# Kernel optimization log

Measured on AMD Instinct MI355X. Metric: run time of the kernel, lower is better.

The kernel has to match this reference:

```python
import jax, jax.numpy as jnp
import numpy as np

N = 8192        # batch_size == num nodes == num hyperedges
D = 512         # hidden_dim
H_HEADS = 8
HD = D // H_HEADS
TOP_K = 16
EPS = 1e-5      # LayerNorm eps


def setup_inputs() -> dict:
    key = jax.random.key(0)
    ks = jax.random.split(key, 10)
    def rn(k, shape, scale=0.02):
        return jax.random.normal(k, shape, dtype=jnp.float32) * scale
    return {
        "x0": jax.random.normal(ks[0], (N, D), dtype=jnp.float32),
        "x1": jax.random.normal(ks[1], (N, D), dtype=jnp.float32),
        # modality projections: Linear -> ReLU -> LayerNorm (per modality)
        "w_p0": rn(ks[2], (D, D)), "b_p0": jnp.zeros((D,), jnp.float32),
        "g0": jnp.ones((D,), jnp.float32), "beta0": jnp.zeros((D,), jnp.float32),
        "w_p1": rn(ks[3], (D, D)), "b_p1": jnp.zeros((D,), jnp.float32),
        "g1": jnp.ones((D,), jnp.float32), "beta1": jnp.zeros((D,), jnp.float32),
        # MultiheadAttention packed in-proj + out-proj
        "in_w": rn(ks[4], (3 * D, D)), "in_b": jnp.zeros((3 * D,), jnp.float32),
        "out_w": rn(ks[5], (D, D)), "out_b": jnp.zeros((D,), jnp.float32),
        # edge weight predictor MLP
        "ew_w1": rn(ks[6], (D // 2, D)), "ew_b1": jnp.zeros((D // 2,), jnp.float32),
        "ew_w2": rn(ks[7], (1, D // 2)), "ew_b2": jnp.zeros((1,), jnp.float32),
    }


def _layernorm(x, g, b):
    m = x.mean(-1, keepdims=True)
    v = ((x - m) ** 2).mean(-1, keepdims=True)
    return (x - m) * jax.lax.rsqrt(v + EPS) * g + b


def _forward(x0, x1, w_p0, b_p0, g0, beta0, w_p1, b_p1, g1, beta1,
             in_w, in_b, out_w, out_b, ew_w1, ew_b1, ew_w2, ew_b2):
    # per-modality projection: Linear -> ReLU -> LayerNorm
    p0 = _layernorm(jax.nn.relu(x0 @ w_p0.T + b_p0), g0, beta0)
    p1 = _layernorm(jax.nn.relu(x1 @ w_p1.T + b_p1), g1, beta1)
    seq = jnp.stack([p0, p1], axis=1)                       # [N, 2, D]
    # cross-modal MHA (self-attention over the 2 modality tokens)
    qkv = seq @ in_w.T + in_b                               # [N, 2, 3D]
    q, k, v = jnp.split(qkv, 3, axis=-1)
    q = q.reshape(N, 2, H_HEADS, HD)
    k = k.reshape(N, 2, H_HEADS, HD)
    v = v.reshape(N, 2, H_HEADS, HD)
    scores = jnp.einsum('bqhd,bkhd->bhqk', q, k) / jnp.sqrt(jnp.float32(HD))
    attn = jax.nn.softmax(scores, axis=-1)                  # [N, h, 2, 2]
    ctx = jnp.einsum('bhqk,bkhd->bqhd', attn, v).reshape(N, 2, D)
    attended = ctx @ out_w.T + out_b                        # [N, 2, D]
    fused = attended.mean(axis=1)                           # [N, D]
    # node-node attention similarity, row-softmax
    sim = jax.nn.softmax(fused @ fused.T, axis=1)           # [N, N]
    _, idx = jax.lax.top_k(sim, TOP_K)                      # [N, K]
    vals = jnp.take_along_axis(sim, idx, axis=1)            # [N, K]
    rows = jnp.arange(N)
    # H[i,i]=1 first, then H[neighbor, i] = sim[i, neighbor] (may overwrite diag)
    H = jnp.zeros((N, N), sim.dtype).at[rows, rows].set(1.0)
    H = H.at[idx, rows[:, None]].set(vals)
    colsum = H.sum(axis=0)
    H = H.at[rows, rows].set(jnp.where(colsum == 0, 1.0, H[rows, rows]))
    # edge weights
    hidden = jax.nn.relu(fused @ ew_w1.T + ew_b1)
    ew = jax.nn.sigmoid(hidden @ ew_w2.T + ew_b2)[:, 0]     # [N]
    ew = jnp.maximum(ew, 1e-8)
    return H, ew


def reference(x0, x1, w_p0, b_p0, g0, beta0, w_p1, b_p1, g1, beta1,
              in_w, in_b, out_w, out_b, ew_w1, ew_b1, ew_w2, ew_b2):
    return _forward(x0, x1, w_p0, b_p0, g0, beta0, w_p1, b_p1, g1, beta1,
                    in_w, in_b, out_w, out_b, ew_w1, ew_b1, ew_w2, ew_b2)
```

## Files before the change

### kernel.cpp

```cpp
#include <hip/hip_runtime.h>
#include <hip/hip_bf16.h>

#define NN 8192
#define DD 512

typedef unsigned short u16;
typedef __bf16 bf16_t;
typedef bf16_t bf16x8 __attribute__((ext_vector_type(8)));
typedef float f32x4 __attribute__((ext_vector_type(4)));

__device__ __forceinline__ float bf2f(u16 h) {
    union { unsigned u; float f; } v; v.u = ((unsigned)h) << 16; return v.f;
}
__device__ __forceinline__ float bflo(unsigned u) {
    union { unsigned u; float f; } v; v.u = u << 16; return v.f;
}
__device__ __forceinline__ float bfhi(unsigned u) {
    union { unsigned u; float f; } v; v.u = u & 0xFFFF0000u; return v.f;
}
__device__ __forceinline__ u16 f2bf(float f) {
    union { float f; unsigned u; } v; v.f = f;
    unsigned r = v.u + 0x7fffu + ((v.u >> 16) & 1u);
    return (u16)(r >> 16);
}

__global__ __launch_bounds__(256) void cvt7(
        const float* __restrict__ s0, u16* __restrict__ d0,
        const float* __restrict__ s1, u16* __restrict__ d1,
        const float* __restrict__ s2, u16* __restrict__ d2,
        const float* __restrict__ s3, u16* __restrict__ d3,
        const float* __restrict__ s4, u16* __restrict__ d4,
        const float* __restrict__ s5, u16* __restrict__ d5,
        const float* __restrict__ s6, u16* __restrict__ d6) {
    size_t v = ((size_t)blockIdx.x * 256 + threadIdx.x) * 8;
    const float* s; u16* d; size_t off;
    if (v < 4194304)      { s = s0; d = d0; off = v; }
    else if (v < 8388608) { s = s1; d = d1; off = v - 4194304; }
    else if (v < 8650752) { s = s2; d = d2; off = v - 8388608; }
    else if (v < 8912896) { s = s3; d = d3; off = v - 8650752; }
    else if (v < 9699328) { s = s4; d = d4; off = v - 8912896; }
    else if (v < 9961472) { s = s5; d = d5; off = v - 9699328; }
    else                  { s = s6; d = d6; off = v - 9961472; }
    float4 a = *(const float4*)(s + off);
    float4 b = *(const float4*)(s + off + 4);
    ushort4 o0 = make_ushort4(f2bf(a.x), f2bf(a.y), f2bf(a.z), f2bf(a.w));
    ushort4 o1 = make_ushort4(f2bf(b.x), f2bf(b.y), f2bf(b.z), f2bf(b.w));
    *(ushort4*)(d + off) = o0;
    *(ushort4*)(d + off + 4) = o1;
}

template<bool RELU, bool BIAS, bool F32OUT>
__global__ __launch_bounds__(256) void gemm_bt(const u16* __restrict__ A,
        const u16* __restrict__ B, const float* __restrict__ bias,
        void* __restrict__ Cv, int M, int Nc, int K) {
    __shared__ alignas(16) u16 As[128 * 32];
    __shared__ alignas(16) u16 Bs[128 * 32];
    const int t = threadIdx.x;
    const int lane = t & 63;
    const int wave = t >> 6;
    const int wm = (wave >> 1) * 64;
    const int wn = (wave & 1) * 64;
    const int rowA = blockIdx.y * 128;
    const int rowB = blockIdx.x * 128;

    f32x4 acc[4][4] = {};

    const int mrow = lane & 15;
    const int kk = (lane >> 4) * 8;

    for (int k0 = 0; k0 < K; k0 += 32) {
        __syncthreads();
        #pragma unroll
        for (int r = 0; r < 2; ++r) {
            int chunk = r * 256 + t;
            const u16* srcA = A + (size_t)(rowA + (chunk >> 2)) * K + k0 + (chunk & 3) * 8;
            __builtin_amdgcn_global_load_lds(
                (const __attribute__((address_space(1))) void*)srcA,
                (__attribute__((address_space(3))) void*)(As + chunk * 8), 16, 0, 0);
            const u16* srcB = B + (size_t)(rowB + (chunk >> 2)) * K + k0 + (chunk & 3) * 8;
            __builtin_amdgcn_global_load_lds(
                (const __attribute__((address_space(1))) void*)srcB,
                (__attribute__((address_space(3))) void*)(Bs + chunk * 8), 16, 0, 0);
        }
        __syncthreads();
        bf16x8 af[4], bfv[4];
        #pragma unroll
        for (int i = 0; i < 4; ++i)
            af[i] = *(const bf16x8*)(As + (wm + i * 16 + mrow) * 32 + kk);
        #pragma unroll
        for (int j = 0; j < 4; ++j)
            bfv[j] = *(const bf16x8*)(Bs + (wn + j * 16 + mrow) * 32 + kk);
        #pragma unroll
        for (int i = 0; i < 4; ++i)
            #pragma unroll
            for (int j = 0; j < 4; ++j)
                acc[i][j] = __builtin_amdgcn_mfma_f32_16x16x32_bf16(af[i], bfv[j], acc[i][j], 0, 0, 0);
    }

    const int crow0 = rowA + wm + (lane >> 4) * 4;
    const int ccol0 = rowB + wn + (lane & 15);
    #pragma unroll
    for (int j = 0; j < 4; ++j) {
        int col = ccol0 + j * 16;
        float bv = BIAS ? bias[col] : 0.0f;
        #pragma unroll
        for (int i = 0; i < 4; ++i) {
            #pragma unroll
            for (int r = 0; r < 4; ++r) {
                float v = acc[i][j][r] + bv;
                if (RELU) v = fmaxf(v, 0.0f);
                size_t off = (size_t)(crow0 + i * 16 + r) * Nc + col;
                if (F32OUT) ((float*)Cv)[off] = v;
                else        ((u16*)Cv)[off] = f2bf(v);
            }
        }
    }
}

__global__ __launch_bounds__(256) void ln_kernel(const u16* __restrict__ y,
        const float* __restrict__ g, const float* __restrict__ b,
        u16* __restrict__ seq, int modality) {
    __shared__ float sred[4];
    int n = blockIdx.x, t = threadIdx.x;
    const u16* yr = y + (size_t)n * DD;
    float x0 = bf2f(yr[t]), x1 = bf2f(yr[t + 256]);
    float s = x0 + x1;
    for (int off = 32; off; off >>= 1) s += __shfl_xor(s, off);
    if ((t & 63) == 0) sred[t >> 6] = s;
    __syncthreads();
    float mean = (sred[0] + sred[1] + sred[2] + sred[3]) * (1.0f / DD);
    __syncthreads();
    float d0 = x0 - mean, d1 = x1 - mean;
    float vs = d0 * d0 + d1 * d1;
    for (int off = 32; off; off >>= 1) vs += __shfl_xor(vs, off);
    if ((t & 63) == 0) sred[t >> 6] = vs;
    __syncthreads();
    float var = (sred[0] + sred[1] + sred[2] + sred[3]) * (1.0f / DD);
    float inv = rsqrtf(var + 1e-5f);
    u16* out = seq + (size_t)n * (2 * DD) + modality * DD;
    out[t]       = f2bf(d0 * inv * g[t]       + b[t]);
    out[t + 256] = f2bf(d1 * inv * g[t + 256] + b[t + 256]);
}

__global__ __launch_bounds__(256) void attn_kernel(const u16* __restrict__ qkv,
        u16* __restrict__ ctxm) {
    int gid = blockIdx.x * 4 + (threadIdx.x >> 6);
    int lane = threadIdx.x & 63;
    int n = gid >> 3, h = gid & 7;
    const u16* r0 = qkv + (size_t)(n * 2) * 1536;
    const u16* r1 = r0 + 1536;
    float q0 = bf2f(r0[h * 64 + lane]);
    float k0 = bf2f(r0[512 + h * 64 + lane]);
    float v0 = bf2f(r0[1024 + h * 64 + lane]);
    float q1 = bf2f(r1[h * 64 + lane]);
    float k1 = bf2f(r1[512 + h * 64 + lane]);
    float v1 = bf2f(r1[1024 + h * 64 + lane]);
    float p00 = q0 * k0, p01 = q0 * k1, p10 = q1 * k0, p11 = q1 * k1;
    for (int off = 32; off; off >>= 1) {
        p00 += __shfl_xor(p00, off);
        p01 += __shfl_xor(p01, off);
        p10 += __shfl_xor(p10, off);
        p11 += __shfl_xor(p11, off);
    }
    const float sc = 0.125f;
    float s00 = p00 * sc, s01 = p01 * sc, s10 = p10 * sc, s11 = p11 * sc;
    float m0 = fmaxf(s00, s01), e00 = __expf(s00 - m0), e01 = __expf(s01 - m0);
    float a00 = e00 / (e00 + e01), a01 = e01 / (e00 + e01);
    float m1 = fmaxf(s10, s11), e10 = __expf(s10 - m1), e11 = __expf(s11 - m1);
    float a10 = e10 / (e10 + e11), a11 = e11 / (e10 + e11);
    float c0 = a00 * v0 + a01 * v1;
    float c1 = a10 * v0 + a11 * v1;
    ctxm[(size_t)n * 512 + h * 64 + lane] = f2bf(0.5f * (c0 + c1));
}

__global__ __launch_bounds__(256) void topk_bf16(const u16* __restrict__ S,
        float* __restrict__ topv, int* __restrict__ topi) {
    const float NEG = -3e38f;
    int row = blockIdx.x * 4 + (threadIdx.x >> 6);
    int lane = threadIdx.x & 63;
    const u16* Sr = S + (size_t)row * NN;

    float m = NEG, l = 0.0f;
    float t1v = NEG, t2v = NEG;
    int t1i = 0x7FFFFFFF, t2i = 0x7FFFFFFF;

    #pragma unroll
    for (int p = 0; p < 16; ++p) {
        uint4 raw = *(const uint4*)(Sr + p * 512 + lane * 8);
        int base = p * 512 + lane * 8;
        #pragma unroll
        for (int q = 0; q < 4; ++q) {
            unsigned w = (&raw.x)[q];
            #pragma unroll
            for (int h = 0; h < 2; ++h) {
                float x = h ? bfhi(w) : bflo(w);
                int xi = base + q * 2 + h;
                if (x > m) { l = l * __expf(m - x) + 1.0f; m = x; }
                else l += __expf(x - m);
                bool g1 = x > t1v, g2 = x > t2v;
                t2v = g1 ? t1v : (g2 ? x : t2v);
                t2i = g1 ? t1i : (g2 ? xi : t2i);
                t1v = g1 ? x : t1v;
                t1i = g1 ? xi : t1i;
            }
        }
    }
    #pragma unroll
    for (int off = 32; off; off >>= 1) {
        float om = __shfl_xor(m, off);
        float ol = __shfl_xor(l, off);
        float nm = fmaxf(m, om);
        l = l * __expf(m - nm) + ol * __expf(om - nm);
        m = nm;
    }

    unsigned mk0 = 0, mk1 = 0, mk2 = 0, mk3 = 0;
    float cv = t1v; int ci = t1i;
    float bv = t2v; int bi = t2i;
    for (int r = 0; r < 16; ++r) {
        float wv = cv; int wi = ci;
        #pragma unroll
        for (int off = 32; off; off >>= 1) {
            float ov = __shfl_xor(wv, off);
            int oi = __shfl_xor(wi, off);
            if (ov > wv || (ov == wv && oi < wi)) { wv = ov; wi = oi; }
        }
        if (lane == 0) {
            topv[(size_t)row * 16 + r] = __expf(wv - m) / l;
            topi[(size_t)row * 16 + r] = wi;
        }
        if (wi == ci) {
            int slot = ((wi >> 9) << 3) | (wi & 7);
            unsigned bit = 1u << (slot & 31);
            if (slot < 32) mk0 |= bit; else if (slot < 64) mk1 |= bit;
            else if (slot < 96) mk2 |= bit; else mk3 |= bit;
            cv = bv; ci = bi;
            bv = NEG; bi = 0x7FFFFFFF;
            if (ci == 0x7FFFFFFF) {
                float nb = NEG; int ni = 0x7FFFFFFF;
                #pragma unroll
                for (int p = 0; p < 16; ++p) {
                    uint4 raw = *(const uint4*)(Sr + p * 512 + lane * 8);
                    int base = p * 512 + lane * 8;
                    #pragma unroll
                    for (int q = 0; q < 4; ++q) {
                        unsigned w = (&raw.x)[q];
                        #pragma unroll
                        for (int h = 0; h < 2; ++h) {
                            int sl = p * 8 + q * 2 + h;
                            unsigned mw = (sl < 32) ? mk0 : (sl < 64) ? mk1
                                        : (sl < 96) ? mk2 : mk3;
                            float x = ((mw >> (sl & 31)) & 1u) ? NEG
                                    : (h ? bfhi(w) : bflo(w));
                            if (x > nb) { nb = x; ni = base + q * 2 + h; }
                        }
                    }
                }
                cv = nb; ci = ni;
            }
        }
    }
}

__global__ __launch_bounds__(256) void diag_kernel(float* __restrict__ H) {
    int i = blockIdx.x * 256 + threadIdx.x;
    H[(size_t)i * NN + i] = 1.0f;
}

__global__ __launch_bounds__(256) void scatter_kernel(const float* __restrict__ topv,
        const int* __restrict__ topi, float* __restrict__ H) {
    int tk = blockIdx.x * 256 + threadIdx.x;
    int i = tk >> 4;
    int idx = topi[tk];
    H[(size_t)idx * NN + i] = topv[tk];
}

__global__ __launch_bounds__(256) void ew_kernel(const u16* __restrict__ hidden,
        const float* __restrict__ w2, const float* __restrict__ b2, float* __restrict__ out) {
    int n = blockIdx.x * 4 + (threadIdx.x >> 6);
    int lane = threadIdx.x & 63;
    const u16* hr = hidden + (size_t)n * 256;
    float s = 0.0f;
    #pragma unroll
    for (int p = 0; p < 4; ++p) s += bf2f(hr[lane + p * 64]) * w2[lane + p * 64];
    for (int off = 32; off; off >>= 1) s += __shfl_xor(s, off);
    if (lane == 0) {
        float z = s + b2[0];
        float sig = 1.0f / (1.0f + __expf(-z));
        out[n] = fmaxf(sig, 1e-8f);
    }
}

extern "C" void kernel_launch(void* const* d_in, const int* in_sizes, int n_in,
                              void* d_out, int out_size, void* d_ws, size_t ws_size,
                              hipStream_t stream) {
    const float* x0    = (const float*)d_in[0];
    const float* x1    = (const float*)d_in[1];
    const float* w_p0  = (const float*)d_in[2];
    const float* b_p0  = (const float*)d_in[3];
    const float* g0    = (const float*)d_in[4];
    const float* beta0 = (const float*)d_in[5];
    const float* w_p1  = (const float*)d_in[6];
    const float* b_p1  = (const float*)d_in[7];
    const float* g1    = (const float*)d_in[8];
    const float* beta1 = (const float*)d_in[9];
    const float* in_w  = (const float*)d_in[10];
    const float* in_b  = (const float*)d_in[11];
    const float* out_w = (const float*)d_in[12];
    const float* out_b = (const float*)d_in[13];
    const float* ew_w1 = (const float*)d_in[14];
    const float* ew_b1 = (const float*)d_in[15];
    const float* ew_w2 = (const float*)d_in[16];
    const float* ew_b2 = (const float*)d_in[17];

    float* Hf = (float*)d_out;
    float* ew_out = Hf + (size_t)NN * NN;

    u16* Hu = (u16*)d_out;
    u16* x0b    = Hu;
    u16* x1b    = Hu + 4194304;
    u16* y0     = Hu + 8388608;
    u16* y1     = Hu + 12582912;
    u16* seq    = Hu + 16777216;
    u16* qkv    = Hu + 25165824;
    u16* ctxm   = Hu + 50331648;
    u16* hidden = Hu + 54525952;
    u16* wp0b   = Hu + 60817408;
    u16* wp1b   = wp0b + 262144;
    u16* inwb   = wp1b + 262144;
    u16* outwb  = inwb + 786432;
    u16* eww1b  = outwb + 262144;
    u16* Sb     = Hu + 67108864;
    char* ws = (char*)d_ws;
    u16* fusedB = (u16*)ws;
    float* topv = (float*)(ws + (8u << 20));
    int*   topi = (int*)(ws + (8u << 20) + 524288);

    dim3 blk(256);
    cvt7<<<dim3(4928), blk, 0, stream>>>(x0, x0b, x1, x1b, w_p0, wp0b, w_p1, wp1b,
                                         in_w, inwb, out_w, outwb, ew_w1, eww1b);
    gemm_bt<true, true, false><<<dim3(4, 64), blk, 0, stream>>>(x0b, wp0b, b_p0, y0, NN, DD, DD);
    gemm_bt<true, true, false><<<dim3(4, 64), blk, 0, stream>>>(x1b, wp1b, b_p1, y1, NN, DD, DD);
    ln_kernel<<<dim3(NN), blk, 0, stream>>>(y0, g0, beta0, seq, 0);
    ln_kernel<<<dim3(NN), blk, 0, stream>>>(y1, g1, beta1, seq, 1);
    gemm_bt<false, true, false><<<dim3(12, 128), blk, 0, stream>>>(seq, inwb, in_b, qkv, 2 * NN, 1536, DD);
    attn_kernel<<<dim3(NN * 8 / 4), blk, 0, stream>>>(qkv, ctxm);
    gemm_bt<false, true, false><<<dim3(4, 64), blk, 0, stream>>>(ctxm, outwb, out_b, fusedB, NN, DD, DD);
    gemm_bt<true, true, false><<<dim3(2, 64), blk, 0, stream>>>(fusedB, eww1b, ew_b1, hidden, NN, 256, DD);
    ew_kernel<<<dim3(NN / 4), blk, 0, stream>>>(hidden, ew_w2, ew_b2, ew_out);
    gemm_bt<false, false, false><<<dim3(64, 64), blk, 0, stream>>>(fusedB, fusedB, nullptr, Sb, NN, NN, DD);
    topk_bf16<<<dim3(NN / 4), blk, 0, stream>>>(Sb, topv, topi);
    hipMemsetAsync(Hf, 0, (size_t)NN * NN * sizeof(float), stream);
    diag_kernel<<<dim3(NN / 256), blk, 0, stream>>>(Hf);
    scatter_kernel<<<dim3(NN * 16 / 256), blk, 0, stream>>>(topv, topi, Hf);
}
```

Measured before the change: 701.0 us.

## Batch modality GEMMs and LayerNorms, deepen GEMM K tile, merge diag with scatter

The two modality projection GEMMs now run as a single launch that picks weights and bias per block-row, and the two LayerNorm launches are merged into one. The GEMM K-step is doubled to 64, which halves the number of barrier-separated iterations at the cost of twice the LDS per block. The diagonal write and the neighbor scatter are fused into one kernel, and the diagonal 1.0 is written only when the node is not among its own top-k. This removes launch overhead and some synchronization. The larger LDS footprint may lower occupancy, and the concurrent scatter/diag writes rely on the skip condition to keep the same overwrite order as before.

New measurement: 702.0 us. About the same (+0.2%).

```diff
diff --git a/kernel.cpp b/kernel.cpp
--- a/kernel.cpp
+++ b/kernel.cpp
@@ -49,12 +49,13 @@
     *(ushort4*)(d + off + 4) = o1;
 }
 
-template<bool RELU, bool BIAS, bool F32OUT>
+template<bool RELU, bool BIAS, bool F32OUT, bool SPLIT>
 __global__ __launch_bounds__(256) void gemm_bt(const u16* __restrict__ A,
         const u16* __restrict__ B, const float* __restrict__ bias,
+        const u16* __restrict__ B2, const float* __restrict__ bias2, int halfY,
         void* __restrict__ Cv, int M, int Nc, int K) {
-    __shared__ alignas(16) u16 As[128 * 32];
-    __shared__ alignas(16) u16 Bs[128 * 32];
+    __shared__ alignas(16) u16 As[128 * 64];
+    __shared__ alignas(16) u16 Bs[128 * 64];
     const int t = threadIdx.x;
     const int lane = t & 63;
     const int wave = t >> 6;
@@ -62,39 +63,43 @@
     const int wn = (wave & 1) * 64;
     const int rowA = blockIdx.y * 128;
     const int rowB = blockIdx.x * 128;
+    if (SPLIT && (int)blockIdx.y >= halfY) { B = B2; bias = bias2; }
 
     f32x4 acc[4][4] = {};
 
     const int mrow = lane & 15;
     const int kk = (lane >> 4) * 8;
 
-    for (int k0 = 0; k0 < K; k0 += 32) {
+    for (int k0 = 0; k0 < K; k0 += 64) {
         __syncthreads();
         #pragma unroll
-        for (int r = 0; r < 2; ++r) {
+        for (int r = 0; r < 4; ++r) {
             int chunk = r * 256 + t;
-            const u16* srcA = A + (size_t)(rowA + (chunk >> 2)) * K + k0 + (chunk & 3) * 8;
+            const u16* srcA = A + (size_t)(rowA + (chunk >> 3)) * K + k0 + (chunk & 7) * 8;
             __builtin_amdgcn_global_load_lds(
                 (const __attribute__((address_space(1))) void*)srcA,
                 (__attribute__((address_space(3))) void*)(As + chunk * 8), 16, 0, 0);
-            const u16* srcB = B + (size_t)(rowB + (chunk >> 2)) * K + k0 + (chunk & 3) * 8;
+            const u16* srcB = B + (size_t)(rowB + (chunk >> 3)) * K + k0 + (chunk & 7) * 8;
             __builtin_amdgcn_global_load_lds(
                 (const __attribute__((address_space(1))) void*)srcB,
                 (__attribute__((address_space(3))) void*)(Bs + chunk * 8), 16, 0, 0);
         }
         __syncthreads();
-        bf16x8 af[4], bfv[4];
-        #pragma unroll
-        for (int i = 0; i < 4; ++i)
-            af[i] = *(const bf16x8*)(As + (wm + i * 16 + mrow) * 32 + kk);
-        #pragma unroll
-        for (int j = 0; j < 4; ++j)
-            bfv[j] = *(const bf16x8*)(Bs + (wn + j * 16 + mrow) * 32 + kk);
-        #pragma unroll
-        for (int i = 0; i < 4; ++i)
+        #pragma unroll
+        for (int ks = 0; ks < 64; ks += 32) {
+            bf16x8 af[4], bfv[4];
+            #pragma unroll
+            for (int i = 0; i < 4; ++i)
+                af[i] = *(const bf16x8*)(As + (wm + i * 16 + mrow) * 64 + ks + kk);
             #pragma unroll
             for (int j = 0; j < 4; ++j)
-                acc[i][j] = __builtin_amdgcn_mfma_f32_16x16x32_bf16(af[i], bfv[j], acc[i][j], 0, 0, 0);
+                bfv[j] = *(const bf16x8*)(Bs + (wn + j * 16 + mrow) * 64 + ks + kk);
+            #pragma unroll
+            for (int i = 0; i < 4; ++i)
+                #pragma unroll
+                for (int j = 0; j < 4; ++j)
+                    acc[i][j] = __builtin_amdgcn_mfma_f32_16x16x32_bf16(af[i], bfv[j], acc[i][j], 0, 0, 0);
+        }
     }
 
     const int crow0 = rowA + wm + (lane >> 4) * 4;
@@ -117,11 +122,15 @@
     }
 }
 
-__global__ __launch_bounds__(256) void ln_kernel(const u16* __restrict__ y,
-        const float* __restrict__ g, const float* __restrict__ b,
-        u16* __restrict__ seq, int modality) {
+__global__ __launch_bounds__(256) void ln2_kernel(const u16* __restrict__ y,
+        const float* __restrict__ g0, const float* __restrict__ b0,
+        const float* __restrict__ g1, const float* __restrict__ b1,
+        u16* __restrict__ seq) {
     __shared__ float sred[4];
     int n = blockIdx.x, t = threadIdx.x;
+    int modality = n >> 13, node = n & (NN - 1);
+    const float* g = modality ? g1 : g0;
+    const float* b = modality ? b1 : b0;
     const u16* yr = y + (size_t)n * DD;
     float x0 = bf2f(yr[t]), x1 = bf2f(yr[t + 256]);
     float s = x0 + x1;
@@ -137,7 +146,7 @@
     __syncthreads();
     float var = (sred[0] + sred[1] + sred[2] + sred[3]) * (1.0f / DD);
     float inv = rsqrtf(var + 1e-5f);
-    u16* out = seq + (size_t)n * (2 * DD) + modality * DD;
+    u16* out = seq + (size_t)node * (2 * DD) + modality * DD;
     out[t]       = f2bf(d0 * inv * g[t]       + b[t]);
     out[t + 256] = f2bf(d1 * inv * g[t + 256] + b[t + 256]);
 }
@@ -262,17 +271,21 @@
     }
 }
 
-__global__ __launch_bounds__(256) void diag_kernel(float* __restrict__ H) {
-    int i = blockIdx.x * 256 + threadIdx.x;
-    H[(size_t)i * NN + i] = 1.0f;
-}
-
-__global__ __launch_bounds__(256) void scatter_kernel(const float* __restrict__ topv,
+__global__ __launch_bounds__(256) void scatter_diag(const float* __restrict__ topv,
         const int* __restrict__ topi, float* __restrict__ H) {
     int tk = blockIdx.x * 256 + threadIdx.x;
-    int i = tk >> 4;
-    int idx = topi[tk];
-    H[(size_t)idx * NN + i] = topv[tk];
+    if (tk < NN * 16) {
+        int i = tk >> 4;
+        int idx = topi[tk];
+        H[(size_t)idx * NN + i] = topv[tk];
+    } else {
+        int c = tk - NN * 16;
+        const int* ti = topi + c * 16;
+        bool self = false;
+        #pragma unroll
+        for (int j = 0; j < 16; ++j) self |= (ti[j] == c);
+        if (!self) H[(size_t)c * NN + c] = 1.0f;
+    }
 }
 
 __global__ __launch_bounds__(256) void ew_kernel(const u16* __restrict__ hidden,
@@ -319,8 +332,7 @@
     u16* Hu = (u16*)d_out;
     u16* x0b    = Hu;
     u16* x1b    = Hu + 4194304;
-    u16* y0     = Hu + 8388608;
-    u16* y1     = Hu + 12582912;
+    u16* y01    = Hu + 8388608;
     u16* seq    = Hu + 16777216;
     u16* qkv    = Hu + 25165824;
     u16* ctxm   = Hu + 50331648;
@@ -337,20 +349,23 @@
     int*   topi = (int*)(ws + (8u << 20) + 524288);
 
     dim3 blk(256);
+    const int BIG = 1 << 30;
     cvt7<<<dim3(4928), blk, 0, stream>>>(x0, x0b, x1, x1b, w_p0, wp0b, w_p1, wp1b,
                                          in_w, inwb, out_w, outwb, ew_w1, eww1b);
-    gemm_bt<true, true, false><<<dim3(4, 64), blk, 0, stream>>>(x0b, wp0b, b_p0, y0, NN, DD, DD);
-    gemm_bt<true, true, false><<<dim3(4, 64), blk, 0, stream>>>(x1b, wp1b, b_p1, y1, NN, DD, DD);
-    ln_kernel<<<dim3(NN), blk, 0, stream>>>(y0, g0, beta0, seq, 0);
-    ln_kernel<<<dim3(NN), blk, 0, stream>>>(y1, g1, beta1, seq, 1);
-    gemm_bt<false, true, false><<<dim3(12, 128), blk, 0, stream>>>(seq, inwb, in_b, qkv, 2 * NN, 1536, DD);
+    gemm_bt<true, true, false, true><<<dim3(4, 128), blk, 0, stream>>>(
+        x0b, wp0b, b_p0, wp1b, b_p1, 64, y01, 2 * NN, DD, DD);
+    ln2_kernel<<<dim3(2 * NN), blk, 0, stream>>>(y01, g0, beta0, g1, beta1, seq);
+    gemm_bt<false, true, false, false><<<dim3(12, 128), blk, 0, stream>>>(
+        seq, inwb, in_b, nullptr, nullptr, BIG, qkv, 2 * NN, 1536, DD);
     attn_kernel<<<dim3(NN * 8 / 4), blk, 0, stream>>>(qkv, ctxm);
-    gemm_bt<false, true, false><<<dim3(4, 64), blk, 0, stream>>>(ctxm, outwb, out_b, fusedB, NN, DD, DD);
-    gemm_bt<true, true, false><<<dim3(2, 64), blk, 0, stream>>>(fusedB, eww1b, ew_b1, hidden, NN, 256, DD);
+    gemm_bt<false, true, false, false><<<dim3(4, 64), blk, 0, stream>>>(
+        ctxm, outwb, out_b, nullptr, nullptr, BIG, fusedB, NN, DD, DD);
+    gemm_bt<true, true, false, false><<<dim3(2, 64), blk, 0, stream>>>(
+        fusedB, eww1b, ew_b1, nullptr, nullptr, BIG, hidden, NN, 256, DD);
     ew_kernel<<<dim3(NN / 4), blk, 0, stream>>>(hidden, ew_w2, ew_b2, ew_out);
-    gemm_bt<false, false, false><<<dim3(64, 64), blk, 0, stream>>>(fusedB, fusedB, nullptr, Sb, NN, NN, DD);
+    gemm_bt<false, false, false, false><<<dim3(64, 64), blk, 0, stream>>>(
+        fusedB, fusedB, nullptr, nullptr, nullptr, BIG, Sb, NN, NN, DD);
     topk_bf16<<<dim3(NN / 4), blk, 0, stream>>>(Sb, topv, topi);
     hipMemsetAsync(Hf, 0, (size_t)NN * NN * sizeof(float), stream);
-    diag_kernel<<<dim3(NN / 256), blk, 0, stream>>>(Hf);
-    scatter_kernel<<<dim3(NN * 16 / 256), blk, 0, stream>>>(topv, topi, Hf);
-}
+    scatter_diag<<<dim3((NN * 16 + NN) / 256), blk, 0, stream>>>(topv, topi, Hf);
+}
```
